# Performance work log

Hardware: AMD Instinct MI355X
Metric: run time of the kernel (lower is better)

The kernel has to match this reference:

```python
import jax, jax.numpy as jnp
import numpy as np

DATA_DIM = 128
UNITS = 512
LAYERS = 3
BATCH = 32
IN_STEPS = 1000   # int((T_input + 0.5*dt)//dt)
OUT_STEPS = 100   # int((T_output + 0.5*dt)//dt)


def setup_inputs() -> dict:
    key = jax.random.key(0)
    ks = jax.random.split(key, 16)
    d = {}
    d["x"] = jax.random.normal(ks[0], (BATCH, IN_STEPS, DATA_DIM), jnp.float32)
    in_dims = [DATA_DIM, UNITS, UNITS]
    i = 1
    for j in range(LAYERS):
        d[f"W{j}"] = jax.random.normal(ks[i], (in_dims[j], 3 * UNITS), jnp.float32) * 0.05; i += 1
        d[f"U{j}"] = jax.random.normal(ks[i], (UNITS, 3 * UNITS), jnp.float32) * 0.05; i += 1
        d[f"b{j}"] = jnp.zeros((2, 3 * UNITS), jnp.float32)
        d[f"s{j}"] = jax.random.normal(ks[i], (1, UNITS), jnp.float32); i += 1
    d["Wd"] = jax.random.normal(ks[i], (UNITS, DATA_DIM), jnp.float32) * 0.05
    d["bd"] = jnp.zeros((DATA_DIM,), jnp.float32)
    return d


def _gru_cell(x, h, W, U, b):
    # Keras GRUCell, reset_after=True (TF2 default)
    mx = x @ W + b[0]           # [B, 3U]
    mh = h @ U + b[1]           # [B, 3U]
    xz, xr, xh = jnp.split(mx, 3, axis=-1)
    hz, hr, hh = jnp.split(mh, 3, axis=-1)
    z = jax.nn.sigmoid(xz + hz)
    r = jax.nn.sigmoid(xr + hr)
    cand = jnp.tanh(xh + r * hh)
    return z * h + (1.0 - z) * cand


def reference(x, W0, U0, b0, s0, W1, U1, b1, s1, W2, U2, b2, s2, Wd, bd):
    params = [(W0, U0, b0), (W1, U1, b1), (W2, U2, b2)]
    B = x.shape[0]
    # learnable initial states, tiled over batch -> [L, B, U]
    h0 = jnp.stack([jnp.tile(s, (B, 1)) for s in (s0, s1, s2)])
    # model processes timesteps 0 .. in_steps-2 (last input step unused)
    xs = jnp.swapaxes(x[:, : IN_STEPS - 1, :], 0, 1)  # [T-1, B, D]

    def step(h, xt):
        hs = []
        inp = xt
        for j, (W, U, b) in enumerate(params):
            hj = _gru_cell(inp, h[j], W, U, b)
            hs.append(hj)
            inp = hj
        hn = jnp.stack(hs)  # [L, B, U]
        return hn, (inp, hn)

    _, (ys, hs) = jax.lax.scan(step, h0, xs)
    # outputs correspond to steps in_steps-out_steps-1 .. in_steps-2
    ys = ys[-OUT_STEPS:]   # [out_steps, B, U]
    hs = hs[-OUT_STEPS:]   # [out_steps, L, B, U]
    preds = ys @ Wd + bd   # [out_steps, B, D]
    predictions = jnp.swapaxes(preds, 0, 1)        # [B, out_steps, D]
    hidden = jnp.transpose(hs, (2, 0, 1, 3))       # [B, out_steps, L, U]
    return predictions, hidden
```

## Files before the change

### kernel.cpp

```cpp
#include <hip/hip_runtime.h>
#include <math.h>

#define B_   32
#define INS  1000
#define TS   999
#define D_   128
#define U_   512
#define G3   1536
#define OUTS 100
#define NB   208
#define NTICK 1002
#define NTHR 512

#define HBUF_OFF 0
#define HBUF_SZ  (2*3*512*32)
#define RING_OFF HBUF_SZ
#define RING_SZ  (4*1536*32)
#define BAR_OFF  (RING_OFF + RING_SZ)

#define W_CHK1  3080
#define W_CHK0  1544
#define XBUF_OFF 12288
#define PART_OFF 24640
#define SMEM_FLOATS 32384
#define PIDX3(q,g,c,e) ((q)*968 + ((g)*8+(c))*40 + (e))

#define WT_STORE(p, v) __hip_atomic_store((p), (v), __ATOMIC_RELAXED, __HIP_MEMORY_SCOPE_AGENT)

#define FMA12() \
  acc[0][0]=fmaf(av.x,w0,acc[0][0]); acc[0][1]=fmaf(av.y,w0,acc[0][1]); \
  acc[0][2]=fmaf(av.z,w0,acc[0][2]); acc[0][3]=fmaf(av.w,w0,acc[0][3]); \
  acc[1][0]=fmaf(av.x,w1,acc[1][0]); acc[1][1]=fmaf(av.y,w1,acc[1][1]); \
  acc[1][2]=fmaf(av.z,w1,acc[1][2]); acc[1][3]=fmaf(av.w,w1,acc[1][3]); \
  acc[2][0]=fmaf(av.x,w2,acc[2][0]); acc[2][1]=fmaf(av.y,w2,acc[2][1]); \
  acc[2][2]=fmaf(av.z,w2,acc[2][2]); acc[2][3]=fmaf(av.w,w2,acc[2][3]);

#define LD16(DST, PTR) { _Pragma("unroll") \
  for (int t_ = 0; t_ < 16; ++t_) DST[t_] = *(const float4*)((PTR) + t_*32); }

#define FMA16(BUF) { _Pragma("unroll") \
  for (int t_ = 0; t_ < 16; ++t_) { \
    const float w0 = wp[0], w1 = wp[1], w2 = wp[2]; \
    const float4 av = BUF[t_]; \
    FMA12(); \
    wp += 24; } }

__global__ void gru_init_kernel(const float* __restrict__ s0,
                                const float* __restrict__ s1,
                                const float* __restrict__ s2,
                                float* __restrict__ ws) {
  int g = blockIdx.x * 256 + threadIdx.x;
  if (g < 1024) { unsigned* bar = (unsigned*)(ws + BAR_OFF); bar[g] = 0u; }
  for (int i = g; i < 3 * 512 * 32; i += gridDim.x * 256) {
    int which = i / (512 * 32);
    int r = i - which * (512 * 32);
    int k = r >> 5, e = r & 31;
    int par = (which == 1) ? 1 : 0;
    const float* s = (which == 0) ? s0 : ((which == 1) ? s1 : s2);
    ws[HBUF_OFF + par * 49152 + which * 16384 + k * 32 + e] = s[k];
  }
}

__device__ __forceinline__ void gbar(unsigned* bar, unsigned ep, int grp) {
  __syncthreads();
  if (threadIdx.x == 0) {
    unsigned lp = __hip_atomic_fetch_add(&bar[64 + grp * 32], 1u,
                                         __ATOMIC_RELAXED, __HIP_MEMORY_SCOPE_AGENT);
    if (lp == ep * 26u - 1u) {
      unsigned rp = __hip_atomic_fetch_add(&bar[32], 1u,
                                           __ATOMIC_RELAXED, __HIP_MEMORY_SCOPE_AGENT);
      if (rp == ep * 8u - 1u) {
        __hip_atomic_store(&bar[0], ep, __ATOMIC_RELAXED, __HIP_MEMORY_SCOPE_AGENT);
      }
    }
    while (__hip_atomic_load(&bar[0], __ATOMIC_RELAXED, __HIP_MEMORY_SCOPE_AGENT) < ep) {
      __builtin_amdgcn_s_sleep(1);
    }
    __builtin_amdgcn_fence(__ATOMIC_ACQUIRE, "agent");
  }
  __syncthreads();
}

__global__ __launch_bounds__(NTHR, 1) void gru_persist(
    const float* __restrict__ x,
    const float* __restrict__ W0c, const float* __restrict__ U0c, const float* __restrict__ b0c,
    const float* __restrict__ W1c, const float* __restrict__ U1c, const float* __restrict__ b1c,
    const float* __restrict__ W2c, const float* __restrict__ U2c, const float* __restrict__ b2c,
    const float* __restrict__ Wd, const float* __restrict__ bd,
    float* __restrict__ out, float* __restrict__ ws)
{
  float* hbuf = ws + HBUF_OFF;
  float* ring = ws + RING_OFF;
  unsigned* bar = (unsigned*)(ws + BAR_OFF);
  float* pred_out = out;
  float* hid_out  = out + B_ * OUTS * D_;

  const int bid = blockIdx.x;
  const int tid = threadIdx.x;
  const int grp = bid & 7;

  int role, rb;
  if      (bid < 16)  { role = -1; rb = bid; }
  else if (bid < 80)  { role = 0;  rb = bid - 16; }
  else if (bid < 144) { role = 1;  rb = bid - 80; }
  else                { role = 2;  rb = bid - 144; }

  __shared__ float smem[SMEM_FLOATS];
  float* part = smem + PART_OFF;

  const int eg  = tid & 7;
  const int c_l = (tid >> 3) & 7;
  const int q   = tid >> 6;
  const int cb  = (rb & 7) * 8 + (rb >> 3);
  const int c0  = cb * 8;
  const int rc = tid >> 5;
  const int re = tid & 31;
  const int xb0 = ((rb & 7) * 2 + (rb >> 3)) * 96;
  const int cg3 = (tid & 31) * 3;
  const int e0  = (tid >> 5) * 2;

  const float *Wj = nullptr, *Ujp = nullptr, *bj = nullptr;
  if      (role == 0) { Ujp = U0c; bj = b0c; }
  else if (role == 1) { Wj = W1c; Ujp = U1c; bj = b1c; }
  else if (role == 2) { Wj = W2c; Ujp = U2c; bj = b2c; }

  if (role < 0) {
    for (int idx = tid; idx < 128 * 96; idx += NTHR)
      smem[idx] = W0c[(idx / 96) * G3 + xb0 + (idx % 96)];
    for (int f = tid; f < 1024; f += NTHR) {
      int e = f >> 5, d4 = (f & 31) * 4;
      *(float4*)(smem + XBUF_OFF + e * 128 + d4) =
          *(const float4*)(x + e * (INS * D_) + d4);
    }
  } else {
    const int chunk = (role == 0) ? 64 : 128;
    const int chks  = (role == 0) ? W_CHK0 : W_CHK1;
    const int total = 8 * chunk * 24;
    for (int idx = tid; idx < total; idx += NTHR) {
      int qq = idx / (chunk * 24);
      int r  = idx - qq * (chunk * 24);
      int i  = r / 24;
      int cg = r - i * 24;
      int c  = cg / 3, g = cg - c * 3;
      const float* mat; int row;
      if (role == 0)      { mat = Ujp; row = qq * 64 + i; }
      else if (qq < 4)    { mat = Wj;  row = qq * 128 + i; }
      else                { mat = Ujp; row = (qq - 4) * 128 + i; }
      smem[qq * chks + (i * 8 + c) * 3 + g] = mat[row * G3 + g * 512 + c0 + c];
    }
  }
  float bz = 0.f, br = 0.f, b0h = 0.f, b1h = 0.f;
  if (role >= 0 && tid < 256) {
    const int cg2 = c0 + rc;
    bz  = bj[cg2] + bj[G3 + cg2];
    br  = bj[512 + cg2] + bj[G3 + 512 + cg2];
    b0h = bj[1024 + cg2];
    b1h = bj[G3 + 1024 + cg2];
  }
  __syncthreads();

  for (int T = 0; T < NTICK; ++T) {
    const int par_prev = (T + 1) & 1;
    const int par_cur  = T & 1;

    if (role < 0) {
      const int t = T;
      if (t < TS) {
        float4 xp0, xp1;
        const bool pf = (t + 1) < TS;
        if (pf) {
          int f0 = tid, f1 = tid + 512;
          xp0 = *(const float4*)(x + (f0 >> 5) * (INS * D_) + (t + 1) * D_ + (f0 & 31) * 4);
          xp1 = *(const float4*)(x + (f1 >> 5) * (INS * D_) + (t + 1) * D_ + (f1 & 31) * 4);
        }
        const float* xb = smem + XBUF_OFF + (t & 1) * 4096;
        float acc[3][2];
        #pragma unroll
        for (int c = 0; c < 3; ++c) { acc[c][0] = 0.f; acc[c][1] = 0.f; }
        #pragma unroll 4
        for (int k4 = 0; k4 < D_; k4 += 4) {
          float4 v0 = *(const float4*)(xb + e0 * 128 + k4);
          float4 v1 = *(const float4*)(xb + (e0 + 1) * 128 + k4);
          float xs0[4] = {v0.x, v0.y, v0.z, v0.w};
          float xs1[4] = {v1.x, v1.y, v1.z, v1.w};
          #pragma unroll
          for (int kk = 0; kk < 4; ++kk) {
            const float* wpx = smem + (k4 + kk) * 96 + cg3;
            float w0 = wpx[0], w1 = wpx[1], w2 = wpx[2];
            acc[0][0] = fmaf(xs0[kk], w0, acc[0][0]);
            acc[0][1] = fmaf(xs1[kk], w0, acc[0][1]);
            acc[1][0] = fmaf(xs0[kk], w1, acc[1][0]);
            acc[1][1] = fmaf(xs1[kk], w1, acc[1][1]);
            acc[2][0] = fmaf(xs0[kk], w2, acc[2][0]);
            acc[2][1] = fmaf(xs1[kk], w2, acc[2][1]);
          }
        }
        float* dst = ring + (t & 3) * (G3 * 32);
        #pragma unroll
        for (int c = 0; c < 3; ++c) {
          WT_STORE(dst + (xb0 + cg3 + c) * 32 + e0,     acc[c][0]);
          WT_STORE(dst + (xb0 + cg3 + c) * 32 + e0 + 1, acc[c][1]);
        }
        if (pf) {
          float* xw = smem + XBUF_OFF + ((t + 1) & 1) * 4096;
          int f0 = tid, f1 = tid + 512;
          *(float4*)(xw + (f0 >> 5) * 128 + (f0 & 31) * 4) = xp0;
          *(float4*)(xw + (f1 >> 5) * 128 + (f1 & 31) * 4) = xp1;
        }
      }
    } else {
      const int j = role;
      const int t = T - (j + 1);
      if (t >= 0 && t < TS) {
        const float* hprev_all = hbuf + par_prev * 49152;
        float xz = 0.f, xr2 = 0.f, xhv0 = 0.f, hp = 0.f;
        if (tid < 256) {
          const int cg2 = c0 + rc;
          hp = hprev_all[j * 16384 + cg2 * 32 + re];
          if (j == 0) {
            const float* r3 = ring + (t & 3) * (G3 * 32);
            xz   = r3[cg2 * 32 + re];
            xr2  = r3[(512 + cg2) * 32 + re];
            xhv0 = r3[(1024 + cg2) * 32 + re];
          }
        }

        float acc[3][4];
        #pragma unroll
        for (int g2 = 0; g2 < 3; ++g2)
          #pragma unroll
          for (int i2 = 0; i2 < 4; ++i2) acc[g2][i2] = 0.f;

        float4 bufA[16], bufB[16], bufC[16];
        if (j == 0) {
          const float* Ab = hprev_all + (q * 64) * 32 + eg * 4;
          const float* wp = smem + q * W_CHK0 + c_l * 3;
          LD16(bufA, Ab);        LD16(bufB, Ab + 512);
          LD16(bufC, Ab + 1024); FMA16(bufA);
          LD16(bufA, Ab + 1536); FMA16(bufB);
          FMA16(bufC);
          FMA16(bufA);
        } else {
          const int kb = (q & 3) * 128;
          const float* Ab = hprev_all + ((q < 4) ? (j - 1) : j) * 16384 + kb * 32 + eg * 4;
          const float* wp = smem + q * W_CHK1 + c_l * 3;
          LD16(bufA, Ab);        LD16(bufB, Ab + 512);
          LD16(bufC, Ab + 1024); FMA16(bufA);
          LD16(bufA, Ab + 1536); FMA16(bufB);
          LD16(bufB, Ab + 2048); FMA16(bufC);
          LD16(bufC, Ab + 2560); FMA16(bufA);
          LD16(bufA, Ab + 3072); FMA16(bufB);
          LD16(bufB, Ab + 3584); FMA16(bufC);
          FMA16(bufA);
          FMA16(bufB);
        }
        #pragma unroll
        for (int g2 = 0; g2 < 3; ++g2) {
          *(float4*)&part[PIDX3(q, g2, c_l, eg * 4)] =
              make_float4(acc[g2][0], acc[g2][1], acc[g2][2], acc[g2][3]);
        }
        __syncthreads();

        if (tid < 256) {
          float gz = 0.f, gr = 0.f, xh = 0.f, hh = 0.f;
          #pragma unroll
          for (int q2 = 0; q2 < 8; ++q2) {
            gz += part[PIDX3(q2, 0, rc, re)];
            gr += part[PIDX3(q2, 1, rc, re)];
            float v = part[PIDX3(q2, 2, rc, re)];
            if (j == 0)       hh += v;
            else if (q2 < 4)  xh += v;
            else              hh += v;
          }
          const int cg2 = c0 + rc;
          const float xhv = (j == 0) ? xhv0 : xh;
          const float zi = gz + xz + bz;
          const float ri = gr + xr2 + br;
          const float z = 1.f / (1.f + expf(-zi));
          const float r = 1.f / (1.f + expf(-ri));
          const float cand = tanhf((xhv + b0h) + r * (hh + b1h));
          const float hn = z * hp + (1.f - z) * cand;
          WT_STORE(&hbuf[par_cur * 49152 + j * 16384 + cg2 * 32 + re], hn);
          if (t >= TS - OUTS) {
            WT_STORE(&hid_out[((re * OUTS + (t - (TS - OUTS))) * 3 + j) * U_ + cg2], hn);
          }
        }
      }
    }
    gbar(bar, (unsigned)(T + 1), grp);
  }

  const int gt = bid * NTHR + tid;
  for (int o = gt; o < B_ * OUTS * D_; o += NB * NTHR) {
    int b  = o / (OUTS * D_);
    int r2 = o - b * (OUTS * D_);
    int s  = r2 >> 7;
    int dd = r2 & 127;
    const float* ys = hid_out + ((b * OUTS + s) * 3 + 2) * U_;
    float acc = bd[dd];
    #pragma unroll 4
    for (int k = 0; k < U_; k += 4) {
      float4 yv = *(const float4*)(ys + k);
      acc = fmaf(yv.x, Wd[(k    ) * D_ + dd], acc);
      acc = fmaf(yv.y, Wd[(k + 1) * D_ + dd], acc);
      acc = fmaf(yv.z, Wd[(k + 2) * D_ + dd], acc);
      acc = fmaf(yv.w, Wd[(k + 3) * D_ + dd], acc);
    }
    pred_out[o] = acc;
  }
}

extern "C" void kernel_launch(void* const* d_in, const int* in_sizes, int n_in,
                              void* d_out, int out_size, void* d_ws, size_t ws_size,
                              hipStream_t stream) {
  const float* x  = (const float*)d_in[0];
  const float* W0 = (const float*)d_in[1];
  const float* U0 = (const float*)d_in[2];
  const float* b0 = (const float*)d_in[3];
  const float* s0 = (const float*)d_in[4];
  const float* W1 = (const float*)d_in[5];
  const float* U1 = (const float*)d_in[6];
  const float* b1 = (const float*)d_in[7];
  const float* s1 = (const float*)d_in[8];
  const float* W2 = (const float*)d_in[9];
  const float* U2 = (const float*)d_in[10];
  const float* b2 = (const float*)d_in[11];
  const float* s2 = (const float*)d_in[12];
  const float* Wd = (const float*)d_in[13];
  const float* bd = (const float*)d_in[14];
  float* ws = (float*)d_ws;

  gru_init_kernel<<<192, 256, 0, stream>>>(s0, s1, s2, ws);
  gru_persist<<<NB, NTHR, 0, stream>>>(x, W0, U0, b0, W1, U1, b1,
                                       W2, U2, b2, Wd, bd, (float*)d_out, ws);
}
```

Baseline: 11.03 ms.

## Fold input projection into layer-0 blocks and drop the dedicated x-projection stage

Removes the 16 blocks that precomputed x@W0 into a global ring buffer. Each layer-0 block now computes its slice of the input projection locally, from a transposed, double-buffered x tile in shared memory with W0 rows appended to its weight slice. This cuts the grid to 192 blocks and the pipeline depth by one tick, and removes the global ring traffic. It also replaces the per-barrier acquire fence with atomic relaxed loads of the hidden state, which adds layer-0 work on the critical path and relies on atomic loads for memory visibility.

```diff
diff --git a/kernel.cpp b/kernel.cpp
--- a/kernel.cpp
+++ b/kernel.cpp
@@ -8,23 +8,35 @@
 #define U_   512
 #define G3   1536
 #define OUTS 100
-#define NB   208
-#define NTICK 1002
+#define NB   192
+#define NTICK 1001
 #define NTHR 512
 
 #define HBUF_OFF 0
 #define HBUF_SZ  (2*3*512*32)
-#define RING_OFF HBUF_SZ
-#define RING_SZ  (4*1536*32)
-#define BAR_OFF  (RING_OFF + RING_SZ)
+#define BAR_OFF  HBUF_SZ
 
 #define W_CHK1  3080
-#define W_CHK0  1544
-#define XBUF_OFF 12288
+#define W_CHK0  1928
+#define XBUF_OFF 15424
 #define PART_OFF 24640
-#define SMEM_FLOATS 32384
+#define XPART_OFF 32384
+#define SMEM_FLOATS 34944
 #define PIDX3(q,g,c,e) ((q)*968 + ((g)*8+(c))*40 + (e))
 
+typedef unsigned long long ull_t;
+
+__device__ __forceinline__ float4 ld_cg16(const float* p) {
+  union { float4 v; ull_t u[2]; } r;
+  r.u[0] = __hip_atomic_load((const ull_t*)p,     __ATOMIC_RELAXED, __HIP_MEMORY_SCOPE_AGENT);
+  r.u[1] = __hip_atomic_load((const ull_t*)p + 1, __ATOMIC_RELAXED, __HIP_MEMORY_SCOPE_AGENT);
+  return r.v;
+}
+__device__ __forceinline__ float ld_cg4(const float* p) {
+  union { float f; unsigned u; } r;
+  r.u = __hip_atomic_load((const unsigned*)p, __ATOMIC_RELAXED, __HIP_MEMORY_SCOPE_AGENT);
+  return r.f;
+}
 #define WT_STORE(p, v) __hip_atomic_store((p), (v), __ATOMIC_RELAXED, __HIP_MEMORY_SCOPE_AGENT)
 
 #define FMA12() \
@@ -35,8 +47,8 @@
   acc[2][0]=fmaf(av.x,w2,acc[2][0]); acc[2][1]=fmaf(av.y,w2,acc[2][1]); \
   acc[2][2]=fmaf(av.z,w2,acc[2][2]); acc[2][3]=fmaf(av.w,w2,acc[2][3]);
 
-#define LD16(DST, PTR) { _Pragma("unroll") \
-  for (int t_ = 0; t_ < 16; ++t_) DST[t_] = *(const float4*)((PTR) + t_*32); }
+#define LDC16(DST, PTR) { _Pragma("unroll") \
+  for (int t_ = 0; t_ < 16; ++t_) DST[t_] = ld_cg16((PTR) + t_*32); }
 
 #define FMA16(BUF) { _Pragma("unroll") \
   for (int t_ = 0; t_ < 16; ++t_) { \
@@ -55,7 +67,7 @@
     int which = i / (512 * 32);
     int r = i - which * (512 * 32);
     int k = r >> 5, e = r & 31;
-    int par = (which == 1) ? 1 : 0;
+    int par = (which == 1) ? 0 : 1;
     const float* s = (which == 0) ? s0 : ((which == 1) ? s1 : s2);
     ws[HBUF_OFF + par * 49152 + which * 16384 + k * 32 + e] = s[k];
   }
@@ -66,7 +78,7 @@
   if (threadIdx.x == 0) {
     unsigned lp = __hip_atomic_fetch_add(&bar[64 + grp * 32], 1u,
                                          __ATOMIC_RELAXED, __HIP_MEMORY_SCOPE_AGENT);
-    if (lp == ep * 26u - 1u) {
+    if (lp == ep * 24u - 1u) {
       unsigned rp = __hip_atomic_fetch_add(&bar[32], 1u,
                                            __ATOMIC_RELAXED, __HIP_MEMORY_SCOPE_AGENT);
       if (rp == ep * 8u - 1u) {
@@ -76,7 +88,6 @@
     while (__hip_atomic_load(&bar[0], __ATOMIC_RELAXED, __HIP_MEMORY_SCOPE_AGENT) < ep) {
       __builtin_amdgcn_s_sleep(1);
     }
-    __builtin_amdgcn_fence(__ATOMIC_ACQUIRE, "agent");
   }
   __syncthreads();
 }
@@ -90,7 +101,6 @@
     float* __restrict__ out, float* __restrict__ ws)
 {
   float* hbuf = ws + HBUF_OFF;
-  float* ring = ws + RING_OFF;
   unsigned* bar = (unsigned*)(ws + BAR_OFF);
   float* pred_out = out;
   float* hid_out  = out + B_ * OUTS * D_;
@@ -99,11 +109,8 @@
   const int tid = threadIdx.x;
   const int grp = bid & 7;
 
-  int role, rb;
-  if      (bid < 16)  { role = -1; rb = bid; }
-  else if (bid < 80)  { role = 0;  rb = bid - 16; }
-  else if (bid < 144) { role = 1;  rb = bid - 80; }
-  else                { role = 2;  rb = bid - 144; }
+  const int role = bid >> 6;
+  const int rb   = bid & 63;
 
   __shared__ float smem[SMEM_FLOATS];
   float* part = smem + PART_OFF;
@@ -115,42 +122,52 @@
   const int c0  = cb * 8;
   const int rc = tid >> 5;
   const int re = tid & 31;
-  const int xb0 = ((rb & 7) * 2 + (rb >> 3)) * 96;
-  const int cg3 = (tid & 31) * 3;
-  const int e0  = (tid >> 5) * 2;
+  const int xe  = tid >> 4;
+  const int xd8 = (tid & 15) * 8;
 
   const float *Wj = nullptr, *Ujp = nullptr, *bj = nullptr;
-  if      (role == 0) { Ujp = U0c; bj = b0c; }
+  if      (role == 0) { Wj = W0c; Ujp = U0c; bj = b0c; }
   else if (role == 1) { Wj = W1c; Ujp = U1c; bj = b1c; }
-  else if (role == 2) { Wj = W2c; Ujp = U2c; bj = b2c; }
-
-  if (role < 0) {
-    for (int idx = tid; idx < 128 * 96; idx += NTHR)
-      smem[idx] = W0c[(idx / 96) * G3 + xb0 + (idx % 96)];
-    for (int f = tid; f < 1024; f += NTHR) {
-      int e = f >> 5, d4 = (f & 31) * 4;
-      *(float4*)(smem + XBUF_OFF + e * 128 + d4) =
-          *(const float4*)(x + e * (INS * D_) + d4);
-    }
-  } else {
-    const int chunk = (role == 0) ? 64 : 128;
-    const int chks  = (role == 0) ? W_CHK0 : W_CHK1;
-    const int total = 8 * chunk * 24;
-    for (int idx = tid; idx < total; idx += NTHR) {
-      int qq = idx / (chunk * 24);
-      int r  = idx - qq * (chunk * 24);
+  else                { Wj = W2c; Ujp = U2c; bj = b2c; }
+
+  if (role == 0) {
+    for (int idx = tid; idx < 8 * 80 * 24; idx += NTHR) {
+      int qq = idx / (80 * 24);
+      int r  = idx - qq * (80 * 24);
       int i  = r / 24;
       int cg = r - i * 24;
       int c  = cg / 3, g = cg - c * 3;
       const float* mat; int row;
-      if (role == 0)      { mat = Ujp; row = qq * 64 + i; }
-      else if (qq < 4)    { mat = Wj;  row = qq * 128 + i; }
-      else                { mat = Ujp; row = (qq - 4) * 128 + i; }
-      smem[qq * chks + (i * 8 + c) * 3 + g] = mat[row * G3 + g * 512 + c0 + c];
+      if (i < 64) { mat = Ujp; row = qq * 64 + i; }
+      else        { mat = Wj;  row = qq * 16 + (i - 64); }
+      smem[qq * W_CHK0 + i * 24 + c * 3 + g] = mat[row * G3 + g * 512 + c0 + c];
+    }
+    {
+      const float* xs = x + xe * (INS * D_) + xd8;
+      union { float4 v; float f[4]; } a, b;
+      a.v = *(const float4*)(xs);
+      b.v = *(const float4*)(xs + 4);
+      #pragma unroll
+      for (int kk = 0; kk < 4; ++kk) {
+        smem[XBUF_OFF + (xd8 + kk) * 32 + xe]     = a.f[kk];
+        smem[XBUF_OFF + (xd8 + 4 + kk) * 32 + xe] = b.f[kk];
+      }
+    }
+  } else {
+    for (int idx = tid; idx < 8 * 128 * 24; idx += NTHR) {
+      int qq = idx / (128 * 24);
+      int r  = idx - qq * (128 * 24);
+      int i  = r / 24;
+      int cg = r - i * 24;
+      int c  = cg / 3, g = cg - c * 3;
+      const float* mat; int row;
+      if (qq < 4) { mat = Wj;  row = qq * 128 + i; }
+      else        { mat = Ujp; row = (qq - 4) * 128 + i; }
+      smem[qq * W_CHK1 + i * 24 + c * 3 + g] = mat[row * G3 + g * 512 + c0 + c];
     }
   }
   float bz = 0.f, br = 0.f, b0h = 0.f, b1h = 0.f;
-  if (role >= 0 && tid < 256) {
+  if (tid < 256) {
     const int cg2 = c0 + rc;
     bz  = bj[cg2] + bj[G3 + cg2];
     br  = bj[512 + cg2] + bj[G3 + 512 + cg2];
@@ -162,103 +179,101 @@
   for (int T = 0; T < NTICK; ++T) {
     const int par_prev = (T + 1) & 1;
     const int par_cur  = T & 1;
-
-    if (role < 0) {
-      const int t = T;
-      if (t < TS) {
-        float4 xp0, xp1;
+    const int j = role;
+    const int t = T - j;
+
+    if (t >= 0 && t < TS) {
+      const float* hprev_all = hbuf + par_prev * 49152;
+      float hp = 0.f;
+      if (tid < 256) hp = ld_cg4(hprev_all + j * 16384 + (c0 + rc) * 32 + re);
+
+      float acc[3][4];
+      #pragma unroll
+      for (int g2 = 0; g2 < 3; ++g2)
+        #pragma unroll
+        for (int i2 = 0; i2 < 4; ++i2) acc[g2][i2] = 0.f;
+
+      if (j == 0) {
+        union { float4 v; float f[4]; } xpa, xpb;
         const bool pf = (t + 1) < TS;
         if (pf) {
-          int f0 = tid, f1 = tid + 512;
-          xp0 = *(const float4*)(x + (f0 >> 5) * (INS * D_) + (t + 1) * D_ + (f0 & 31) * 4);
-          xp1 = *(const float4*)(x + (f1 >> 5) * (INS * D_) + (t + 1) * D_ + (f1 & 31) * 4);
-        }
-        const float* xb = smem + XBUF_OFF + (t & 1) * 4096;
-        float acc[3][2];
+          const float* xs = x + xe * (INS * D_) + (t + 1) * D_ + xd8;
+          xpa.v = *(const float4*)(xs);
+          xpb.v = *(const float4*)(xs + 4);
+        }
+        float accX[4] = {0.f, 0.f, 0.f, 0.f};
+        const float* Ab = hprev_all + (q * 64) * 32 + eg * 4;
+        const float* wp = smem + q * W_CHK0 + c_l * 3;
+        float4 bufA[16], bufB[16], bufC[16];
+        LDC16(bufA, Ab);        LDC16(bufB, Ab + 512);
+        LDC16(bufC, Ab + 1024); FMA16(bufA);
+        LDC16(bufA, Ab + 1536); FMA16(bufB);
+        FMA16(bufC);
+        FMA16(bufA);
+        const float* xbq = smem + XBUF_OFF + (t & 1) * 4096 + (q * 16) * 32 + eg * 4;
         #pragma unroll
-        for (int c = 0; c < 3; ++c) { acc[c][0] = 0.f; acc[c][1] = 0.f; }
-        #pragma unroll 4
-        for (int k4 = 0; k4 < D_; k4 += 4) {
-          float4 v0 = *(const float4*)(xb + e0 * 128 + k4);
-          float4 v1 = *(const float4*)(xb + (e0 + 1) * 128 + k4);
-          float xs0[4] = {v0.x, v0.y, v0.z, v0.w};
-          float xs1[4] = {v1.x, v1.y, v1.z, v1.w};
+        for (int i = 0; i < 16; ++i) {
+          const float4 av = *(const float4*)(xbq + i * 32);
+          const float w0 = wp[0], w1 = wp[1], w2 = wp[2];
+          acc[0][0]=fmaf(av.x,w0,acc[0][0]); acc[0][1]=fmaf(av.y,w0,acc[0][1]);
+          acc[0][2]=fmaf(av.z,w0,acc[0][2]); acc[0][3]=fmaf(av.w,w0,acc[0][3]);
+          acc[1][0]=fmaf(av.x,w1,acc[1][0]); acc[1][1]=fmaf(av.y,w1,acc[1][1]);
+          acc[1][2]=fmaf(av.z,w1,acc[1][2]); acc[1][3]=fmaf(av.w,w1,acc[1][3]);
+          accX[0]=fmaf(av.x,w2,accX[0]); accX[1]=fmaf(av.y,w2,accX[1]);
+          accX[2]=fmaf(av.z,w2,accX[2]); accX[3]=fmaf(av.w,w2,accX[3]);
+          wp += 24;
+        }
+        #pragma unroll
+        for (int g2 = 0; g2 < 3; ++g2)
+          *(float4*)&part[PIDX3(q, g2, c_l, eg * 4)] =
+              make_float4(acc[g2][0], acc[g2][1], acc[g2][2], acc[g2][3]);
+        *(float4*)&smem[XPART_OFF + q * 320 + c_l * 40 + eg * 4] =
+            make_float4(accX[0], accX[1], accX[2], accX[3]);
+        __syncthreads();
+
+        if (tid < 256) {
+          float gz = 0.f, gr = 0.f, hh = 0.f, xh = 0.f;
+          #pragma unroll
+          for (int q2 = 0; q2 < 8; ++q2) {
+            gz += part[PIDX3(q2, 0, rc, re)];
+            gr += part[PIDX3(q2, 1, rc, re)];
+            hh += part[PIDX3(q2, 2, rc, re)];
+            xh += smem[XPART_OFF + q2 * 320 + rc * 40 + re];
+          }
+          const int cg2 = c0 + rc;
+          const float z = 1.f / (1.f + expf(-(gz + bz)));
+          const float r = 1.f / (1.f + expf(-(gr + br)));
+          const float cand = tanhf((xh + b0h) + r * (hh + b1h));
+          const float hn = z * hp + (1.f - z) * cand;
+          WT_STORE(&hbuf[par_cur * 49152 + 0 * 16384 + cg2 * 32 + re], hn);
+          if (t >= TS - OUTS)
+            WT_STORE(&hid_out[((re * OUTS + (t - (TS - OUTS))) * 3 + 0) * U_ + cg2], hn);
+        }
+        if (pf) {
+          float* xw = smem + XBUF_OFF + ((t + 1) & 1) * 4096;
           #pragma unroll
           for (int kk = 0; kk < 4; ++kk) {
-            const float* wpx = smem + (k4 + kk) * 96 + cg3;
-            float w0 = wpx[0], w1 = wpx[1], w2 = wpx[2];
-            acc[0][0] = fmaf(xs0[kk], w0, acc[0][0]);
-            acc[0][1] = fmaf(xs1[kk], w0, acc[0][1]);
-            acc[1][0] = fmaf(xs0[kk], w1, acc[1][0]);
-            acc[1][1] = fmaf(xs1[kk], w1, acc[1][1]);
-            acc[2][0] = fmaf(xs0[kk], w2, acc[2][0]);
-            acc[2][1] = fmaf(xs1[kk], w2, acc[2][1]);
+            xw[(xd8 + kk) * 32 + xe]     = xpa.f[kk];
+            xw[(xd8 + 4 + kk) * 32 + xe] = xpb.f[kk];
           }
         }
-        float* dst = ring + (t & 3) * (G3 * 32);
-        #pragma unroll
-        for (int c = 0; c < 3; ++c) {
-          WT_STORE(dst + (xb0 + cg3 + c) * 32 + e0,     acc[c][0]);
-          WT_STORE(dst + (xb0 + cg3 + c) * 32 + e0 + 1, acc[c][1]);
-        }
-        if (pf) {
-          float* xw = smem + XBUF_OFF + ((t + 1) & 1) * 4096;
-          int f0 = tid, f1 = tid + 512;
-          *(float4*)(xw + (f0 >> 5) * 128 + (f0 & 31) * 4) = xp0;
-          *(float4*)(xw + (f1 >> 5) * 128 + (f1 & 31) * 4) = xp1;
-        }
-      }
-    } else {
-      const int j = role;
-      const int t = T - (j + 1);
-      if (t >= 0 && t < TS) {
-        const float* hprev_all = hbuf + par_prev * 49152;
-        float xz = 0.f, xr2 = 0.f, xhv0 = 0.f, hp = 0.f;
-        if (tid < 256) {
-          const int cg2 = c0 + rc;
-          hp = hprev_all[j * 16384 + cg2 * 32 + re];
-          if (j == 0) {
-            const float* r3 = ring + (t & 3) * (G3 * 32);
-            xz   = r3[cg2 * 32 + re];
-            xr2  = r3[(512 + cg2) * 32 + re];
-            xhv0 = r3[(1024 + cg2) * 32 + re];
-          }
-        }
-
-        float acc[3][4];
+      } else {
+        const float* Ab = hprev_all + ((q < 4) ? (j - 1) : j) * 16384 + ((q & 3) * 128) * 32 + eg * 4;
+        const float* wp = smem + q * W_CHK1 + c_l * 3;
+        float4 bufA[16], bufB[16], bufC[16];
+        LDC16(bufA, Ab);        LDC16(bufB, Ab + 512);
+        LDC16(bufC, Ab + 1024); FMA16(bufA);
+        LDC16(bufA, Ab + 1536); FMA16(bufB);
+        LDC16(bufB, Ab + 2048); FMA16(bufC);
+        LDC16(bufC, Ab + 2560); FMA16(bufA);
+        LDC16(bufA, Ab + 3072); FMA16(bufB);
+        LDC16(bufB, Ab + 3584); FMA16(bufC);
+        FMA16(bufA);
+        FMA16(bufB);
         #pragma unroll
         for (int g2 = 0; g2 < 3; ++g2)
-          #pragma unroll
-          for (int i2 = 0; i2 < 4; ++i2) acc[g2][i2] = 0.f;
-
-        float4 bufA[16], bufB[16], bufC[16];
-        if (j == 0) {
-          const float* Ab = hprev_all + (q * 64) * 32 + eg * 4;
-          const float* wp = smem + q * W_CHK0 + c_l * 3;
-          LD16(bufA, Ab);        LD16(bufB, Ab + 512);
-          LD16(bufC, Ab + 1024); FMA16(bufA);
-          LD16(bufA, Ab + 1536); FMA16(bufB);
-          FMA16(bufC);
-          FMA16(bufA);
-        } else {
-          const int kb = (q & 3) * 128;
-          const float* Ab = hprev_all + ((q < 4) ? (j - 1) : j) * 16384 + kb * 32 + eg * 4;
-          const float* wp = smem + q * W_CHK1 + c_l * 3;
-          LD16(bufA, Ab);        LD16(bufB, Ab + 512);
-          LD16(bufC, Ab + 1024); FMA16(bufA);
-          LD16(bufA, Ab + 1536); FMA16(bufB);
-          LD16(bufB, Ab + 2048); FMA16(bufC);
-          LD16(bufC, Ab + 2560); FMA16(bufA);
-          LD16(bufA, Ab + 3072); FMA16(bufB);
-          LD16(bufB, Ab + 3584); FMA16(bufC);
-          FMA16(bufA);
-          FMA16(bufB);
-        }
-        #pragma unroll
-        for (int g2 = 0; g2 < 3; ++g2) {
           *(float4*)&part[PIDX3(q, g2, c_l, eg * 4)] =
               make_float4(acc[g2][0], acc[g2][1], acc[g2][2], acc[g2][3]);
-        }
         __syncthreads();
 
         if (tid < 256) {
@@ -268,27 +283,23 @@
             gz += part[PIDX3(q2, 0, rc, re)];
             gr += part[PIDX3(q2, 1, rc, re)];
             float v = part[PIDX3(q2, 2, rc, re)];
-            if (j == 0)       hh += v;
-            else if (q2 < 4)  xh += v;
-            else              hh += v;
+            if (q2 < 4) xh += v; else hh += v;
           }
           const int cg2 = c0 + rc;
-          const float xhv = (j == 0) ? xhv0 : xh;
-          const float zi = gz + xz + bz;
-          const float ri = gr + xr2 + br;
-          const float z = 1.f / (1.f + expf(-zi));
-          const float r = 1.f / (1.f + expf(-ri));
-          const float cand = tanhf((xhv + b0h) + r * (hh + b1h));
+          const float z = 1.f / (1.f + expf(-(gz + bz)));
+          const float r = 1.f / (1.f + expf(-(gr + br)));
+          const float cand = tanhf((xh + b0h) + r * (hh + b1h));
           const float hn = z * hp + (1.f - z) * cand;
           WT_STORE(&hbuf[par_cur * 49152 + j * 16384 + cg2 * 32 + re], hn);
-          if (t >= TS - OUTS) {
+          if (t >= TS - OUTS)
             WT_STORE(&hid_out[((re * OUTS + (t - (TS - OUTS))) * 3 + j) * U_ + cg2], hn);
-          }
         }
       }
     }
     gbar(bar, (unsigned)(T + 1), grp);
   }
+
+  __builtin_amdgcn_fence(__ATOMIC_ACQUIRE, "agent");
 
   const int gt = bid * NTHR + tid;
   for (int o = gt; o < B_ * OUTS * D_; o += NB * NTHR) {
```

After: 19.76 ms. 1.79x slower.

## Double threads per block and split the K reduction across sixteen slices

Applied to the files above, without the earlier changes.

Raises the block size from 512 to 1024 threads, so each recurrent block splits its matrix-vector reduction into 16 K-slices instead of 8, halving the serial FMA chain per thread. Weight staging in shared memory is re-laid out into the smaller chunks, and the partial-sum reduction now runs over 16 slices. The x-projection blocks use the extra threads for the input prefetch, with a barrier added before the prefetched tile is written. This aims to shorten per-tick latency on the serial recurrence, at the cost of more shared-memory partials, a longer final reduction and a higher register-pressure limit per thread.

```diff
diff --git a/kernel.cpp b/kernel.cpp
--- a/kernel.cpp
+++ b/kernel.cpp
@@ -10,7 +10,7 @@
 #define OUTS 100
 #define NB   208
 #define NTICK 1002
-#define NTHR 512
+#define NTHR 1024
 
 #define HBUF_OFF 0
 #define HBUF_SZ  (2*3*512*32)
@@ -18,11 +18,11 @@
 #define RING_SZ  (4*1536*32)
 #define BAR_OFF  (RING_OFF + RING_SZ)
 
-#define W_CHK1  3080
-#define W_CHK0  1544
+#define W_CHK1  1544
+#define W_CHK0  776
 #define XBUF_OFF 12288
-#define PART_OFF 24640
-#define SMEM_FLOATS 32384
+#define PART_OFF 24704
+#define SMEM_FLOATS 40192
 #define PIDX3(q,g,c,e) ((q)*968 + ((g)*8+(c))*40 + (e))
 
 #define WT_STORE(p, v) __hip_atomic_store((p), (v), __ATOMIC_RELAXED, __HIP_MEMORY_SCOPE_AGENT)
@@ -118,6 +118,8 @@
   const int xb0 = ((rb & 7) * 2 + (rb >> 3)) * 96;
   const int cg3 = (tid & 31) * 3;
   const int e0  = (tid >> 5) * 2;
+  const int xe  = tid >> 5;
+  const int xd4 = (tid & 31) * 4;
 
   const float *Wj = nullptr, *Ujp = nullptr, *bj = nullptr;
   if      (role == 0) { Ujp = U0c; bj = b0c; }
@@ -127,26 +129,28 @@
   if (role < 0) {
     for (int idx = tid; idx < 128 * 96; idx += NTHR)
       smem[idx] = W0c[(idx / 96) * G3 + xb0 + (idx % 96)];
-    for (int f = tid; f < 1024; f += NTHR) {
-      int e = f >> 5, d4 = (f & 31) * 4;
-      *(float4*)(smem + XBUF_OFF + e * 128 + d4) =
-          *(const float4*)(x + e * (INS * D_) + d4);
+    *(float4*)(smem + XBUF_OFF + xe * 128 + xd4) =
+        *(const float4*)(x + xe * (INS * D_) + xd4);
+  } else if (role == 0) {
+    for (int idx = tid; idx < 16 * 32 * 24; idx += NTHR) {
+      int qq = idx / (32 * 24);
+      int r  = idx - qq * (32 * 24);
+      int i  = r / 24;
+      int cg = r - i * 24;
+      int c  = cg / 3, g = cg - c * 3;
+      smem[qq * W_CHK0 + i * 24 + c * 3 + g] = Ujp[(qq * 32 + i) * G3 + g * 512 + c0 + c];
     }
   } else {
-    const int chunk = (role == 0) ? 64 : 128;
-    const int chks  = (role == 0) ? W_CHK0 : W_CHK1;
-    const int total = 8 * chunk * 24;
-    for (int idx = tid; idx < total; idx += NTHR) {
-      int qq = idx / (chunk * 24);
-      int r  = idx - qq * (chunk * 24);
+    for (int idx = tid; idx < 16 * 64 * 24; idx += NTHR) {
+      int qq = idx / (64 * 24);
+      int r  = idx - qq * (64 * 24);
       int i  = r / 24;
       int cg = r - i * 24;
       int c  = cg / 3, g = cg - c * 3;
       const float* mat; int row;
-      if (role == 0)      { mat = Ujp; row = qq * 64 + i; }
-      else if (qq < 4)    { mat = Wj;  row = qq * 128 + i; }
-      else                { mat = Ujp; row = (qq - 4) * 128 + i; }
-      smem[qq * chks + (i * 8 + c) * 3 + g] = mat[row * G3 + g * 512 + c0 + c];
+      if (qq < 8) { mat = Wj;  row = qq * 64 + i; }
+      else        { mat = Ujp; row = (qq - 8) * 64 + i; }
+      smem[qq * W_CHK1 + i * 24 + c * 3 + g] = mat[row * G3 + g * 512 + c0 + c];
     }
   }
   float bz = 0.f, br = 0.f, b0h = 0.f, b1h = 0.f;
@@ -166,46 +170,43 @@
     if (role < 0) {
       const int t = T;
       if (t < TS) {
-        float4 xp0, xp1;
+        float4 xp;
         const bool pf = (t + 1) < TS;
+        if (pf)
+          xp = *(const float4*)(x + xe * (INS * D_) + (t + 1) * D_ + xd4);
+        if (tid < 512) {
+          const float* xb = smem + XBUF_OFF + (t & 1) * 4096;
+          float acc[3][2];
+          #pragma unroll
+          for (int c = 0; c < 3; ++c) { acc[c][0] = 0.f; acc[c][1] = 0.f; }
+          #pragma unroll 4
+          for (int k4 = 0; k4 < D_; k4 += 4) {
+            float4 v0 = *(const float4*)(xb + e0 * 128 + k4);
+            float4 v1 = *(const float4*)(xb + (e0 + 1) * 128 + k4);
+            float xs0[4] = {v0.x, v0.y, v0.z, v0.w};
+            float xs1[4] = {v1.x, v1.y, v1.z, v1.w};
+            #pragma unroll
+            for (int kk = 0; kk < 4; ++kk) {
+              const float* wpx = smem + (k4 + kk) * 96 + cg3;
+              float w0 = wpx[0], w1 = wpx[1], w2 = wpx[2];
+              acc[0][0] = fmaf(xs0[kk], w0, acc[0][0]);
+              acc[0][1] = fmaf(xs1[kk], w0, acc[0][1]);
+              acc[1][0] = fmaf(xs0[kk], w1, acc[1][0]);
+              acc[1][1] = fmaf(xs1[kk], w1, acc[1][1]);
+              acc[2][0] = fmaf(xs0[kk], w2, acc[2][0]);
+              acc[2][1] = fmaf(xs1[kk], w2, acc[2][1]);
+            }
+          }
+          float* dst = ring + (t & 3) * (G3 * 32);
+          #pragma unroll
+          for (int c = 0; c < 3; ++c) {
+            WT_STORE(dst + (xb0 + cg3 + c) * 32 + e0,     acc[c][0]);
+            WT_STORE(dst + (xb0 + cg3 + c) * 32 + e0 + 1, acc[c][1]);
+          }
+        }
         if (pf) {
-          int f0 = tid, f1 = tid + 512;
-          xp0 = *(const float4*)(x + (f0 >> 5) * (INS * D_) + (t + 1) * D_ + (f0 & 31) * 4);
-          xp1 = *(const float4*)(x + (f1 >> 5) * (INS * D_) + (t + 1) * D_ + (f1 & 31) * 4);
-        }
-        const float* xb = smem + XBUF_OFF + (t & 1) * 4096;
-        float acc[3][2];
-        #pragma unroll
-        for (int c = 0; c < 3; ++c) { acc[c][0] = 0.f; acc[c][1] = 0.f; }
-        #pragma unroll 4
-        for (int k4 = 0; k4 < D_; k4 += 4) {
-          float4 v0 = *(const float4*)(xb + e0 * 128 + k4);
-          float4 v1 = *(const float4*)(xb + (e0 + 1) * 128 + k4);
-          float xs0[4] = {v0.x, v0.y, v0.z, v0.w};
-          float xs1[4] = {v1.x, v1.y, v1.z, v1.w};
-          #pragma unroll
-          for (int kk = 0; kk < 4; ++kk) {
-            const float* wpx = smem + (k4 + kk) * 96 + cg3;
-            float w0 = wpx[0], w1 = wpx[1], w2 = wpx[2];
-            acc[0][0] = fmaf(xs0[kk], w0, acc[0][0]);
-            acc[0][1] = fmaf(xs1[kk], w0, acc[0][1]);
-            acc[1][0] = fmaf(xs0[kk], w1, acc[1][0]);
-            acc[1][1] = fmaf(xs1[kk], w1, acc[1][1]);
-            acc[2][0] = fmaf(xs0[kk], w2, acc[2][0]);
-            acc[2][1] = fmaf(xs1[kk], w2, acc[2][1]);
-          }
-        }
-        float* dst = ring + (t & 3) * (G3 * 32);
-        #pragma unroll
-        for (int c = 0; c < 3; ++c) {
-          WT_STORE(dst + (xb0 + cg3 + c) * 32 + e0,     acc[c][0]);
-          WT_STORE(dst + (xb0 + cg3 + c) * 32 + e0 + 1, acc[c][1]);
-        }
-        if (pf) {
-          float* xw = smem + XBUF_OFF + ((t + 1) & 1) * 4096;
-          int f0 = tid, f1 = tid + 512;
-          *(float4*)(xw + (f0 >> 5) * 128 + (f0 & 31) * 4) = xp0;
-          *(float4*)(xw + (f1 >> 5) * 128 + (f1 & 31) * 4) = xp1;
+          __syncthreads();
+          *(float4*)(smem + XBUF_OFF + ((t + 1) & 1) * 4096 + xe * 128 + xd4) = xp;
         }
       }
     } else {
@@ -233,43 +234,35 @@
 
         float4 bufA[16], bufB[16], bufC[16];
         if (j == 0) {
-          const float* Ab = hprev_all + (q * 64) * 32 + eg * 4;
+          const float* Ab = hprev_all + q * 1024 + eg * 4;
           const float* wp = smem + q * W_CHK0 + c_l * 3;
+          LD16(bufA, Ab); LD16(bufB, Ab + 512);
+          FMA16(bufA);
+          FMA16(bufB);
+        } else {
+          const float* Ab = hprev_all + ((q < 8) ? (j - 1) : j) * 16384 + ((q & 7) * 64) * 32 + eg * 4;
+          const float* wp = smem + q * W_CHK1 + c_l * 3;
           LD16(bufA, Ab);        LD16(bufB, Ab + 512);
           LD16(bufC, Ab + 1024); FMA16(bufA);
           LD16(bufA, Ab + 1536); FMA16(bufB);
           FMA16(bufC);
           FMA16(bufA);
-        } else {
-          const int kb = (q & 3) * 128;
-          const float* Ab = hprev_all + ((q < 4) ? (j - 1) : j) * 16384 + kb * 32 + eg * 4;
-          const float* wp = smem + q * W_CHK1 + c_l * 3;
-          LD16(bufA, Ab);        LD16(bufB, Ab + 512);
-          LD16(bufC, Ab + 1024); FMA16(bufA);
-          LD16(bufA, Ab + 1536); FMA16(bufB);
-          LD16(bufB, Ab + 2048); FMA16(bufC);
-          LD16(bufC, Ab + 2560); FMA16(bufA);
-          LD16(bufA, Ab + 3072); FMA16(bufB);
-          LD16(bufB, Ab + 3584); FMA16(bufC);
-          FMA16(bufA);
-          FMA16(bufB);
         }
         #pragma unroll
-        for (int g2 = 0; g2 < 3; ++g2) {
+        for (int g2 = 0; g2 < 3; ++g2)
           *(float4*)&part[PIDX3(q, g2, c_l, eg * 4)] =
               make_float4(acc[g2][0], acc[g2][1], acc[g2][2], acc[g2][3]);
-        }
         __syncthreads();
 
         if (tid < 256) {
           float gz = 0.f, gr = 0.f, xh = 0.f, hh = 0.f;
           #pragma unroll
-          for (int q2 = 0; q2 < 8; ++q2) {
+          for (int q2 = 0; q2 < 16; ++q2) {
             gz += part[PIDX3(q2, 0, rc, re)];
             gr += part[PIDX3(q2, 1, rc, re)];
             float v = part[PIDX3(q2, 2, rc, re)];
             if (j == 0)       hh += v;
-            else if (q2 < 4)  xh += v;
+            else if (q2 < 8)  xh += v;
             else              hh += v;
           }
           const int cg2 = c0 + rc;
```

After: 12.65 ms. +14.7%, slower.
